# Performance work log

Measured on AMD Instinct MI355X. Metric: run time of the kernel, lower is better.

The kernel has to match this reference:

```python
import jax, jax.numpy as jnp
import numpy as np

B, S, H, FF, E = 4, 4096, 1024, 4096, 8
EPS = 1e-5


def setup_inputs() -> dict:
    key = jax.random.key(0)
    ks = jax.random.split(key, 8)
    std = 0.02
    return {
        "x": jax.random.normal(ks[0], (B, S, H), jnp.float32),
        "norm_weight": jnp.ones((H,), jnp.float32),
        "router_w": jax.random.normal(ks[1], (E, H), jnp.float32) * std,
        "router_b": jnp.zeros((E,), jnp.float32),
        "fc1_w": jax.random.normal(ks[2], (E, FF, H), jnp.float32) * std,
        "fc1_b": jnp.zeros((E, FF), jnp.float32),
        "fc2_w": jax.random.normal(ks[3], (E, H, FF), jnp.float32) * std,
        "fc2_b": jnp.zeros((E, H), jnp.float32),
    }


def reference(x, norm_weight, router_w, router_b, fc1_w, fc1_b, fc2_w, fc2_b):
    b, s, h = x.shape
    T = b * s
    e = router_w.shape[0]
    cap = T // e  # expert capacity, capacity_factor = 1.0

    x_flat = x.reshape(T, h)
    # RMSNorm (pre-norm on MoE input)
    xn = x_flat * jax.lax.rsqrt(jnp.mean(x_flat * x_flat, axis=-1, keepdims=True) + EPS) * norm_weight

    # Router (no jitter: eval / jitter_noise=0)
    logits = xn @ router_w.T + router_b          # [T, E]
    probs = jax.nn.softmax(logits, axis=-1)       # [T, E]

    # Expert-choice routing: each expert picks its top-`cap` tokens by prob
    gates, idx = jax.lax.top_k(probs.T, cap)      # [E, cap], [E, cap]

    # Dispatch (gather) and grouped expert MLP
    xe = xn[idx]                                   # [E, cap, H]
    hmid = jnp.einsum('ech,efh->ecf', xe, fc1_w) + fc1_b[:, None, :]
    hmid = jax.nn.gelu(hmid, approximate=False)    # torch F.gelu default (exact)
    ye = jnp.einsum('ecf,ehf->ech', hmid, fc2_w) + fc2_b[:, None, :]

    # Combine: gated scatter-add back to token positions, normalize by gate sum
    flat_idx = idx.reshape(-1)                     # [E*cap]
    weighted = (ye * gates[..., None]).reshape(-1, h)
    out = jnp.zeros((T, h), x.dtype).at[flat_idx].add(weighted)
    gate_sums = jnp.zeros((T, 1), x.dtype).at[flat_idx].add(gates.reshape(-1, 1))
    out = out / jnp.maximum(gate_sums, 1e-9)       # unrouted tokens stay zero
    return out.reshape(b, s, h)
```

## Files before the change

### kernel.cpp

```cpp
#include <hip/hip_runtime.h>
#include <hip/hip_bf16.h>

#define T_TOK 16384
#define H_DIM 1024
#define FF_DIM 4096
#define NE 8
#define CAP 2048
#define EPS_F 1e-5f

#define BM2 256
#define BN2 256
#define BK2 32

typedef __attribute__((ext_vector_type(4))) float f32x4;
typedef __attribute__((ext_vector_type(8))) short bf16x8;
typedef unsigned long long u64;
typedef unsigned int u32;

__device__ inline void gload_lds16(const void* g, void* l) {
  __builtin_amdgcn_global_load_lds(
      (const __attribute__((address_space(1))) unsigned int*)g,
      (__attribute__((address_space(3))) unsigned int*)l, 16, 0, 0);
}

__device__ inline unsigned short bf16_bits(float f) {
  __hip_bfloat16 h = __float2bfloat16(f);
  unsigned short u;
  __builtin_memcpy(&u, &h, 2);
  return u;
}

__device__ inline float bits_f32(unsigned short u) {
  const u32 x = ((u32)u) << 16;
  float f;
  __builtin_memcpy(&f, &x, 4);
  return f;
}

__global__ __launch_bounds__(256) void router_kernel(
    const float* __restrict__ x, const float* __restrict__ nw,
    const float* __restrict__ rw, const float* __restrict__ rb,
    __hip_bfloat16* __restrict__ xn, u64* __restrict__ keys,
    int* __restrict__ tok_cnt,
    const float* __restrict__ w1s, __hip_bfloat16* __restrict__ w1d,
    const float* __restrict__ w2s, __hip_bfloat16* __restrict__ w2d, int do_cvt) {
  const int t = blockIdx.x;
  const int tid = threadIdx.x;
  if (tid == 0) tok_cnt[t] = 0;
  const float4 v = reinterpret_cast<const float4*>(x + (size_t)t * H_DIM)[tid];
  float ss = v.x * v.x + v.y * v.y + v.z * v.z + v.w * v.w;
#pragma unroll
  for (int o = 32; o > 0; o >>= 1) ss += __shfl_down(ss, o);
  __shared__ float red[4];
  __shared__ float redl[4][NE];
  const int wv = tid >> 6, ln = tid & 63;
  if (ln == 0) red[wv] = ss;
  __syncthreads();
  const float tot = red[0] + red[1] + red[2] + red[3];
  const float scale = rsqrtf(tot * (1.0f / H_DIM) + EPS_F);
  const float4 w4 = reinterpret_cast<const float4*>(nw)[tid];
  float xv0 = v.x * scale * w4.x, xv1 = v.y * scale * w4.y;
  float xv2 = v.z * scale * w4.z, xv3 = v.w * scale * w4.w;
  ushort4 u4;
  u4.x = bf16_bits(xv0); u4.y = bf16_bits(xv1);
  u4.z = bf16_bits(xv2); u4.w = bf16_bits(xv3);
  reinterpret_cast<ushort4*>(xn + (size_t)t * H_DIM)[tid] = u4;
  float lg[NE];
#pragma unroll
  for (int e = 0; e < NE; ++e) {
    const float4 r4 = reinterpret_cast<const float4*>(rw + (size_t)e * H_DIM)[tid];
    lg[e] = xv0 * r4.x + xv1 * r4.y + xv2 * r4.z + xv3 * r4.w;
  }
#pragma unroll
  for (int o = 32; o > 0; o >>= 1) {
#pragma unroll
    for (int e = 0; e < NE; ++e) lg[e] += __shfl_down(lg[e], o);
  }
  if (ln == 0) {
#pragma unroll
    for (int e = 0; e < NE; ++e) redl[wv][e] = lg[e];
  }
  __syncthreads();
  if (tid == 0) {
    float l[NE];
    float m = -1e30f;
#pragma unroll
    for (int e = 0; e < NE; ++e) {
      l[e] = redl[0][e] + redl[1][e] + redl[2][e] + redl[3][e] + rb[e];
      m = fmaxf(m, l[e]);
    }
    float s = 0.f;
#pragma unroll
    for (int e = 0; e < NE; ++e) { l[e] = expf(l[e] - m); s += l[e]; }
    const float inv = 1.0f / s;
#pragma unroll
    for (int e = 0; e < NE; ++e) {
      const float p = l[e] * inv;
      const u64 key = ((u64)__float_as_uint(p) << 32) | (u32)(0xFFFFFFFFu - (u32)t);
      keys[(size_t)e * T_TOK + t] = key;
    }
  }
  if (do_cvt) {
    const int n4each = NE * FF_DIM * H_DIM / 4;
    const int gstride = gridDim.x * blockDim.x;
    for (int i = blockIdx.x * blockDim.x + tid; i < 2 * n4each; i += gstride) {
      const float* s = (i < n4each) ? w1s : w2s;
      __hip_bfloat16* d = (i < n4each) ? w1d : w2d;
      const int j = (i < n4each) ? i : i - n4each;
      const float4 vv = reinterpret_cast<const float4*>(s)[j];
      ushort4 o;
      o.x = bf16_bits(vv.x); o.y = bf16_bits(vv.y);
      o.z = bf16_bits(vv.z); o.w = bf16_bits(vv.w);
      reinterpret_cast<ushort4*>(d)[j] = o;
    }
  }
}

#define EQCAP 7168
__global__ __launch_bounds__(1024) void topk_kernel(
    const u64* __restrict__ keys, int* __restrict__ idxl,
    float* __restrict__ gatel, int* __restrict__ tok_list, int* __restrict__ tok_cnt) {
  const int e = blockIdx.x;
  const int tid = threadIdx.x;
  const int lane = tid & 63;
  const u64* ke = keys + (size_t)e * T_TOK;
  __shared__ int hist[256];
  __shared__ u32 s_pref;
  __shared__ int s_k;
  __shared__ int s_cnt;
  __shared__ int s_eq;
  __shared__ u32 eqlist[EQCAP];

  u32 pref = 0;
  int pbits = 0;
  int kneed = CAP;
  for (int pass = 0; pass < 4; ++pass) {
    if (tid < 256) hist[tid] = 0;
    __syncthreads();
    const int shift = 24 - 8 * pass;
    for (int i = tid; i < T_TOK; i += 1024) {
      const u32 hi = (u32)(ke[i] >> 32);
      const bool ok = (pbits == 0) || ((hi >> (32 - pbits)) == pref);
      const int d = ok ? (int)((hi >> shift) & 255) : -1;
      u64 act = __ballot(ok);
      while (act) {
        const int src = __ffsll((long long)act) - 1;
        const int dl = __shfl(d, src);
        const u64 mb = __ballot(ok && (d == dl));
        if (lane == src) atomicAdd(&hist[dl], (int)__popcll(mb));
        act &= ~mb;
      }
    }
    __syncthreads();
    if (tid == 0) {
      int cum = 0;
      int d = 255;
      for (; d >= 0; --d) {
        cum += hist[d];
        if (cum >= kneed) break;
      }
      s_k = kneed - (cum - hist[d]);
      s_pref = (pref << 8) | (u32)d;
    }
    __syncthreads();
    pref = s_pref;
    kneed = s_k;
    pbits += 8;
    __syncthreads();
  }
  const u32 thrp = pref;
  const float thrp_f = __uint_as_float(thrp);

  if (tid == 0) { s_cnt = 0; s_eq = 0; }
  __syncthreads();
  for (int i = tid; i < T_TOK; i += 1024) {
    const u64 key = ke[i];
    const u32 hi = (u32)(key >> 32);
    if (hi > thrp) {
      const int pos = atomicAdd(&s_cnt, 1);
      if (pos < CAP) {
        const int tok = (int)(0xFFFFFFFFu - (u32)key);
        idxl[e * CAP + pos] = tok;
        gatel[e * CAP + pos] = __uint_as_float(hi);
        const int j = atomicAdd(tok_cnt + tok, 1);
        if (j < NE) tok_list[tok * NE + j] = e * CAP + pos;
      }
    } else if (hi == thrp) {
      const int j = atomicAdd(&s_eq, 1);
      if (j < EQCAP) eqlist[j] = (u32)key;
    }
  }
  __syncthreads();
  const int neq = s_eq;
  if (neq <= EQCAP) {
    u32 prefl = 0;
    int pb = 0;
    int kn = kneed;
    if (neq > kneed) {
      for (int pass = 0; pass < 4; ++pass) {
        if (tid < 256) hist[tid] = 0;
        __syncthreads();
        const int shift = 24 - 8 * pass;
        for (int i = tid; i < neq; i += 1024) {
          const u32 vv = eqlist[i];
          if ((pb == 0) || ((vv >> (32 - pb)) == prefl)) atomicAdd(&hist[(vv >> shift) & 255], 1);
        }
        __syncthreads();
        if (tid == 0) {
          int cum = 0;
          int d = 255;
          for (; d >= 0; --d) {
            cum += hist[d];
            if (cum >= kn) break;
          }
          s_k = kn - (cum - hist[d]);
          s_pref = (prefl << 8) | (u32)d;
        }
        __syncthreads();
        prefl = s_pref;
        kn = s_k;
        pb += 8;
        __syncthreads();
      }
    }
    for (int i = tid; i < neq; i += 1024) {
      const u32 lo = eqlist[i];
      if (neq <= kneed || lo >= prefl) {
        const int pos = atomicAdd(&s_cnt, 1);
        if (pos < CAP) {
          const int tok = (int)(0xFFFFFFFFu - lo);
          idxl[e * CAP + pos] = tok;
          gatel[e * CAP + pos] = thrp_f;
          const int j = atomicAdd(tok_cnt + tok, 1);
          if (j < NE) tok_list[tok * NE + j] = e * CAP + pos;
        }
      }
    }
  } else {
    u64 pref64 = (u64)thrp;
    int pb64 = 32;
    int kn = kneed;
    for (int pass = 4; pass < 8; ++pass) {
      if (tid < 256) hist[tid] = 0;
      __syncthreads();
      const int shift = 56 - 8 * pass;
      for (int i = tid; i < T_TOK; i += 1024) {
        const u64 key = ke[i];
        if ((key >> (64 - pb64)) == pref64) atomicAdd(&hist[(int)((key >> shift) & 255)], 1);
      }
      __syncthreads();
      if (tid == 0) {
        int cum = 0;
        int d = 255;
        for (; d >= 0; --d) {
          cum += hist[d];
          if (cum >= kn) break;
        }
        s_k = kn - (cum - hist[d]);
        s_pref = (u32)d;
      }
      __syncthreads();
      pref64 = (pref64 << 8) | s_pref;
      kn = s_k;
      pb64 += 8;
      __syncthreads();
    }
    for (int i = tid; i < T_TOK; i += 1024) {
      const u64 key = ke[i];
      if ((u32)(key >> 32) == thrp && key >= pref64) {
        const int pos = atomicAdd(&s_cnt, 1);
        if (pos < CAP) {
          const int tok = (int)(0xFFFFFFFFu - (u32)key);
          idxl[e * CAP + pos] = tok;
          gatel[e * CAP + pos] = thrp_f;
          const int j = atomicAdd(tok_cnt + tok, 1);
          if (j < NE) tok_list[tok * NE + j] = e * CAP + pos;
        }
      }
    }
  }
}

__global__ __launch_bounds__(256) void cvt2_kernel(
    const float* __restrict__ s1, __hip_bfloat16* __restrict__ d1,
    const float* __restrict__ s2, __hip_bfloat16* __restrict__ d2, int n4each) {
  int i = blockIdx.x * blockDim.x + threadIdx.x;
  const int stride = gridDim.x * blockDim.x;
  for (; i < 2 * n4each; i += stride) {
    const float* s = (i < n4each) ? s1 : s2;
    __hip_bfloat16* d = (i < n4each) ? d1 : d2;
    const int j = (i < n4each) ? i : i - n4each;
    const float4 v = reinterpret_cast<const float4*>(s)[j];
    ushort4 o;
    o.x = bf16_bits(v.x); o.y = bf16_bits(v.y);
    o.z = bf16_bits(v.z); o.w = bf16_bits(v.w);
    reinterpret_cast<ushort4*>(d)[j] = o;
  }
}

template <int MODE>
__global__ __launch_bounds__(1024) void gemm7_kernel(
    const __hip_bfloat16* __restrict__ Asrc, const __hip_bfloat16* __restrict__ Bw,
    const float* __restrict__ bias, const int* __restrict__ idxl,
    const float* __restrict__ gatel, __hip_bfloat16* __restrict__ hmid,
    __hip_bfloat16* __restrict__ ye, int ebase) {
  constexpr int N = (MODE == 0) ? FF_DIM : H_DIM;
  constexpr int K = (MODE == 0) ? H_DIM : FF_DIM;
  constexpr int NBN = N / BN2;
  constexpr int LOG_NBN = (MODE == 0) ? 4 : 2;
  constexpr int BPE = (CAP / BM2) * NBN;
  constexpr int LOG_BPE = (MODE == 0) ? 7 : 5;
  constexpr int NT = K / BK2;

  const int nwg = gridDim.x;
  const int wg0 = blockIdx.x;
  const int wg = (wg0 & 7) * (nwg >> 3) + (wg0 >> 3);
  const int z = wg >> LOG_BPE;
  const int rr = wg & (BPE - 1);
  const int bm = rr >> LOG_NBN;
  const int bn = rr & (NBN - 1);
  const int e = ebase + z;

  const int tid = threadIdx.x;
  const int lane = tid & 63;
  const int w = tid >> 6;
  const int wr = w >> 2, wc = w & 3;
  const int fr = lane & 15, q = lane >> 4;

  __shared__ char smem[131072];

  const int srow = tid >> 2;
  const int sg = tid & 3;
  const int skoff = (sg ^ ((srow >> 1) & 3)) * 8;

  const __hip_bfloat16* asrc;
  if constexpr (MODE == 0) {
    const int t0 = idxl[e * CAP + bm * BM2 + srow];
    asrc = Asrc + (size_t)t0 * H_DIM + skoff;
  } else {
    asrc = Asrc + ((size_t)z * CAP + bm * BM2 + srow) * FF_DIM + skoff;
  }
  const __hip_bfloat16* bsrc = Bw + (size_t)z * N * K + (size_t)(bn * BN2 + srow) * K + skoff;

  const int slotk = ((q ^ ((fr >> 1) & 3)) << 4);
  const int aoff0 = (wr * 64 + fr) * 64 + slotk;
  const int boff0 = 16384 + (wc * 64 + fr) * 64 + slotk;

  f32x4 acc[4][4] = {};
  bf16x8 Af[4], Bf[4];

#define GLDA(sb, k0) gload_lds16(asrc + (k0), smem + (sb)*32768 + tid * 16)
#define GLDB(sb, k0) gload_lds16(bsrc + (k0), smem + (sb)*32768 + 16384 + tid * 16)

  GLDA(0, 0); GLDB(0, 0);
  GLDA(1, BK2); GLDB(1, BK2);
  GLDA(2, 2 * BK2); GLDB(2, 2 * BK2);
  asm volatile("s_waitcnt vmcnt(4)");
  __builtin_amdgcn_s_barrier();
  __builtin_amdgcn_sched_barrier(0);

  for (int kt = 0; kt < NT; ++kt) {
    const int cur = kt & 3;
    const int kref = (kt + 3 < NT) ? (kt + 3) : (kt + 3 - NT);
    const int k0p = kref * BK2;
    const int psl = (kt + 3) & 3;
    const char* base = smem + cur * 32768;

    Af[0] = *reinterpret_cast<const bf16x8*>(base + aoff0);
    Af[1] = *reinterpret_cast<const bf16x8*>(base + aoff0 + 1024);
    Af[2] = *reinterpret_cast<const bf16x8*>(base + aoff0 + 2048);
    Af[3] = *reinterpret_cast<const bf16x8*>(base + aoff0 + 3072);
    Bf[0] = *reinterpret_cast<const bf16x8*>(base + boff0);
    Bf[1] = *reinterpret_cast<const bf16x8*>(base + boff0 + 1024);
    __builtin_amdgcn_sched_barrier(0);
    Bf[2] = *reinterpret_cast<const bf16x8*>(base + boff0 + 2048);
    Bf[3] = *reinterpret_cast<const bf16x8*>(base + boff0 + 3072);
    GLDA(psl, k0p);
    asm volatile("s_waitcnt vmcnt(3)");
    __builtin_amdgcn_s_barrier();
    asm volatile("s_waitcnt lgkmcnt(2)");
    __builtin_amdgcn_sched_barrier(0);
    __builtin_amdgcn_s_setprio(1);
#pragma unroll
    for (int m_ = 0; m_ < 4; ++m_) {
      acc[m_][0] = __builtin_amdgcn_mfma_f32_16x16x32_bf16(Af[m_], Bf[0], acc[m_][0], 0, 0, 0);
      acc[m_][1] = __builtin_amdgcn_mfma_f32_16x16x32_bf16(Af[m_], Bf[1], acc[m_][1], 0, 0, 0);
    }
    __builtin_amdgcn_s_setprio(0);
    __builtin_amdgcn_sched_barrier(0);

    GLDB(psl, k0p);
    asm volatile("s_waitcnt lgkmcnt(0)");
    __builtin_amdgcn_sched_barrier(0);
    __builtin_amdgcn_s_barrier();
    __builtin_amdgcn_sched_barrier(0);
    __builtin_amdgcn_s_setprio(1);
#pragma unroll
    for (int m_ = 0; m_ < 4; ++m_) {
      acc[m_][2] = __builtin_amdgcn_mfma_f32_16x16x32_bf16(Af[m_], Bf[2], acc[m_][2], 0, 0, 0);
      acc[m_][3] = __builtin_amdgcn_mfma_f32_16x16x32_bf16(Af[m_], Bf[3], acc[m_][3], 0, 0, 0);
    }
    __builtin_amdgcn_s_setprio(0);
    __builtin_amdgcn_sched_barrier(0);
  }
#undef GLDA
#undef GLDB

  if constexpr (MODE == 0) {
#pragma unroll
    for (int m = 0; m < 4; ++m) {
      const int rbase = bm * BM2 + wr * 64 + m * 16 + q * 4;
#pragma unroll
      for (int n = 0; n < 4; ++n) {
        const int gn = bn * BN2 + wc * 64 + n * 16 + fr;
        const float bb = bias[e * FF_DIM + gn];
#pragma unroll
        for (int i = 0; i < 4; ++i) {
          const float v = acc[m][n][i] + bb;
          const float u = v * (1.5957691216f + 0.0713548162972f * v * v);
          const float s = 1.0f / (1.0f + __expf(-u));
          hmid[((size_t)z * CAP + rbase + i) * FF_DIM + gn] = __float2bfloat16(v * s);
        }
      }
    }
  } else {
#pragma unroll
    for (int m = 0; m < 4; ++m) {
      const int rbase = bm * BM2 + wr * 64 + m * 16 + q * 4;
      float gt[4];
#pragma unroll
      for (int i = 0; i < 4; ++i) gt[i] = gatel[e * CAP + rbase + i];
#pragma unroll
      for (int n = 0; n < 4; ++n) {
        const int gn = bn * BN2 + wc * 64 + n * 16 + fr;
        const float bb = bias[e * H_DIM + gn];
#pragma unroll
        for (int i = 0; i < 4; ++i)
          ye[((size_t)e * CAP + rbase + i) * H_DIM + gn] =
              __float2bfloat16((acc[m][n][i] + bb) * gt[i]);
      }
    }
  }
}

__global__ __launch_bounds__(256) void combine_kernel(
    const __hip_bfloat16* __restrict__ ye, const float* __restrict__ gatel,
    const int* __restrict__ tok_list, const int* __restrict__ tok_cnt,
    float* __restrict__ out) {
  const int t = blockIdx.x;
  const int tid = threadIdx.x;
  const int cnt = tok_cnt[t];
  float a0 = 0.f, a1 = 0.f, a2 = 0.f, a3 = 0.f, gs = 0.f;
  for (int j = 0; j < cnt && j < NE; ++j) {
    const int ent = tok_list[t * NE + j];
    gs += gatel[ent];
    const ushort4 v = reinterpret_cast<const ushort4*>(ye + (size_t)ent * H_DIM)[tid];
    a0 += bits_f32(v.x);
    a1 += bits_f32(v.y);
    a2 += bits_f32(v.z);
    a3 += bits_f32(v.w);
  }
  const float inv = 1.0f / fmaxf(gs, 1e-9f);
  float4 o;
  o.x = a0 * inv; o.y = a1 * inv; o.z = a2 * inv; o.w = a3 * inv;
  reinterpret_cast<float4*>(out + (size_t)t * H_DIM)[tid] = o;
}

extern "C" void kernel_launch(void* const* d_in, const int* in_sizes, int n_in,
                              void* d_out, int out_size, void* d_ws, size_t ws_size,
                              hipStream_t stream) {
  const float* x = (const float*)d_in[0];
  const float* nw = (const float*)d_in[1];
  const float* rw = (const float*)d_in[2];
  const float* rb = (const float*)d_in[3];
  const float* fc1w = (const float*)d_in[4];
  const float* fc1b = (const float*)d_in[5];
  const float* fc2w = (const float*)d_in[6];
  const float* fc2b = (const float*)d_in[7];
  float* out = (float*)d_out;

  char* ws = (char*)d_ws;
  size_t off = 0;
  auto alloc = [&](size_t b) {
    char* p = ws + off;
    off += (b + 255) & ~(size_t)255;
    return p;
  };
  __hip_bfloat16* xn = (__hip_bfloat16*)alloc((size_t)T_TOK * H_DIM * 2);
  u64* keys = (u64*)alloc((size_t)NE * T_TOK * 8);
  int* idxl = (int*)alloc((size_t)NE * CAP * 4);
  float* gatel = (float*)alloc((size_t)NE * CAP * 4);
  int* tok_list = (int*)alloc((size_t)T_TOK * NE * 4);
  int* tok_cnt = (int*)alloc((size_t)T_TOK * 4);
  __hip_bfloat16* ye = (__hip_bfloat16*)alloc((size_t)NE * CAP * H_DIM * 2);

  int EC = NE;
  while (EC > 1) {
    const size_t per = (size_t)EC * ((size_t)FF_DIM * H_DIM * 2 * 2 + (size_t)CAP * FF_DIM * 2);
    if (off + per + 4096 <= ws_size) break;
    EC >>= 1;
  }
  __hip_bfloat16* w1b = (__hip_bfloat16*)alloc((size_t)EC * FF_DIM * H_DIM * 2);
  __hip_bfloat16* w2b = (__hip_bfloat16*)alloc((size_t)EC * H_DIM * FF_DIM * 2);
  __hip_bfloat16* hmid = (__hip_bfloat16*)alloc((size_t)EC * CAP * FF_DIM * 2);

  const int fused_cvt = (EC == NE) ? 1 : 0;

  router_kernel<<<T_TOK, 256, 0, stream>>>(x, nw, rw, rb, xn, keys, tok_cnt,
                                           fc1w, w1b, fc2w, w2b, fused_cvt);
  topk_kernel<<<NE, 1024, 0, stream>>>(keys, idxl, gatel, tok_list, tok_cnt);

  for (int eb = 0; eb < NE; eb += EC) {
    if (!fused_cvt) {
      const int n4 = EC * FF_DIM * H_DIM / 4;
      cvt2_kernel<<<4096, 256, 0, stream>>>(fc1w + (size_t)eb * FF_DIM * H_DIM, w1b,
                                            fc2w + (size_t)eb * H_DIM * FF_DIM, w2b, n4);
    }
    const int nb1 = EC * (CAP / BM2) * (FF_DIM / BN2);
    gemm7_kernel<0><<<nb1, 1024, 0, stream>>>(xn, w1b, fc1b, idxl, gatel, hmid, ye, eb);
    const int nb2 = EC * (CAP / BM2) * (H_DIM / BN2);
    gemm7_kernel<1><<<nb2, 1024, 0, stream>>>(hmid, w2b, fc2b, idxl, gatel, hmid, ye, eb);
  }
  combine_kernel<<<T_TOK, 256, 0, stream>>>(ye, gatel, tok_list, tok_cnt, out);
}
```

Before: 505.3 us.

## Shrink expert GEMM tiles to 256x128 with 512 threads and triple-buffered LDS

Replaces the 1024-thread 256x256 expert GEMM with a 512-thread 256x128 tile. Each thread now loads two A rows per stage, and the LDS ring drops from four stages to three, cutting shared memory to 72KB. The aim is to run more workgroups per CU and launch twice as many blocks, which should improve latency hiding and load balance. In exchange, each B tile is reused across fewer columns, so more global traffic goes to the A operand, and the shallower prefetch may expose more memory latency.

```diff
diff --git a/kernel.cpp b/kernel.cpp
--- a/kernel.cpp
+++ b/kernel.cpp
@@ -8,8 +8,8 @@
 #define CAP 2048
 #define EPS_F 1e-5f
 
-#define BM2 256
-#define BN2 256
+#define BM3 256
+#define BN3 128
 #define BK2 32
 
 typedef __attribute__((ext_vector_type(4))) float f32x4;
@@ -299,17 +299,17 @@
 }
 
 template <int MODE>
-__global__ __launch_bounds__(1024) void gemm7_kernel(
+__global__ __launch_bounds__(512, 4) void gemm10_kernel(
     const __hip_bfloat16* __restrict__ Asrc, const __hip_bfloat16* __restrict__ Bw,
     const float* __restrict__ bias, const int* __restrict__ idxl,
     const float* __restrict__ gatel, __hip_bfloat16* __restrict__ hmid,
     __hip_bfloat16* __restrict__ ye, int ebase) {
   constexpr int N = (MODE == 0) ? FF_DIM : H_DIM;
   constexpr int K = (MODE == 0) ? H_DIM : FF_DIM;
-  constexpr int NBN = N / BN2;
-  constexpr int LOG_NBN = (MODE == 0) ? 4 : 2;
-  constexpr int BPE = (CAP / BM2) * NBN;
-  constexpr int LOG_BPE = (MODE == 0) ? 7 : 5;
+  constexpr int NBN = N / BN3;
+  constexpr int LOG_NBN = (MODE == 0) ? 5 : 3;
+  constexpr int BPE = (CAP / BM3) * NBN;
+  constexpr int LOG_BPE = (MODE == 0) ? 8 : 6;
   constexpr int NT = K / BK2;
 
   const int nwg = gridDim.x;
@@ -324,23 +324,27 @@
   const int tid = threadIdx.x;
   const int lane = tid & 63;
   const int w = tid >> 6;
-  const int wr = w >> 2, wc = w & 3;
+  const int wr = w >> 1, wc = w & 1;
   const int fr = lane & 15, q = lane >> 4;
 
-  __shared__ char smem[131072];
+  __shared__ char smem[73728];
 
   const int srow = tid >> 2;
   const int sg = tid & 3;
   const int skoff = (sg ^ ((srow >> 1) & 3)) * 8;
 
-  const __hip_bfloat16* asrc;
+  const __hip_bfloat16* asrc0;
+  const __hip_bfloat16* asrc1;
   if constexpr (MODE == 0) {
-    const int t0 = idxl[e * CAP + bm * BM2 + srow];
-    asrc = Asrc + (size_t)t0 * H_DIM + skoff;
+    const int t0 = idxl[e * CAP + bm * BM3 + srow];
+    const int t1 = idxl[e * CAP + bm * BM3 + 128 + srow];
+    asrc0 = Asrc + (size_t)t0 * H_DIM + skoff;
+    asrc1 = Asrc + (size_t)t1 * H_DIM + skoff;
   } else {
-    asrc = Asrc + ((size_t)z * CAP + bm * BM2 + srow) * FF_DIM + skoff;
-  }
-  const __hip_bfloat16* bsrc = Bw + (size_t)z * N * K + (size_t)(bn * BN2 + srow) * K + skoff;
+    asrc0 = Asrc + ((size_t)z * CAP + bm * BM3 + srow) * FF_DIM + skoff;
+    asrc1 = asrc0 + (size_t)128 * FF_DIM;
+  }
+  const __hip_bfloat16* bsrc = Bw + (size_t)z * N * K + (size_t)(bn * BN3 + srow) * K + skoff;
 
   const int slotk = ((q ^ ((fr >> 1) & 3)) << 4);
   const int aoff0 = (wr * 64 + fr) * 64 + slotk;
@@ -349,22 +353,26 @@
   f32x4 acc[4][4] = {};
   bf16x8 Af[4], Bf[4];
 
-#define GLDA(sb, k0) gload_lds16(asrc + (k0), smem + (sb)*32768 + tid * 16)
-#define GLDB(sb, k0) gload_lds16(bsrc + (k0), smem + (sb)*32768 + 16384 + tid * 16)
+#define GLDA(sb, k0)                                            \
+  do {                                                          \
+    char* d_ = smem + (sb)*24576 + tid * 16;                    \
+    gload_lds16(asrc0 + (k0), d_);                              \
+    gload_lds16(asrc1 + (k0), d_ + 8192);                       \
+  } while (0)
+#define GLDB(sb, k0) gload_lds16(bsrc + (k0), smem + (sb)*24576 + 16384 + tid * 16)
 
   GLDA(0, 0); GLDB(0, 0);
   GLDA(1, BK2); GLDB(1, BK2);
-  GLDA(2, 2 * BK2); GLDB(2, 2 * BK2);
-  asm volatile("s_waitcnt vmcnt(4)");
+  asm volatile("s_waitcnt vmcnt(3)");
   __builtin_amdgcn_s_barrier();
   __builtin_amdgcn_sched_barrier(0);
 
   for (int kt = 0; kt < NT; ++kt) {
-    const int cur = kt & 3;
-    const int kref = (kt + 3 < NT) ? (kt + 3) : (kt + 3 - NT);
+    const int cur = kt % 3;
+    const int psl = (kt + 2) % 3;
+    const int kref = (kt + 2 < NT) ? (kt + 2) : (kt + 2 - NT);
     const int k0p = kref * BK2;
-    const int psl = (kt + 3) & 3;
-    const char* base = smem + cur * 32768;
+    const char* base = smem + cur * 24576;
 
     Af[0] = *reinterpret_cast<const bf16x8*>(base + aoff0);
     Af[1] = *reinterpret_cast<const bf16x8*>(base + aoff0 + 1024);
@@ -376,7 +384,7 @@
     Bf[2] = *reinterpret_cast<const bf16x8*>(base + boff0 + 2048);
     Bf[3] = *reinterpret_cast<const bf16x8*>(base + boff0 + 3072);
     GLDA(psl, k0p);
-    asm volatile("s_waitcnt vmcnt(3)");
+    asm volatile("s_waitcnt vmcnt(2)");
     __builtin_amdgcn_s_barrier();
     asm volatile("s_waitcnt lgkmcnt(2)");
     __builtin_amdgcn_sched_barrier(0);
@@ -409,10 +417,10 @@
   if constexpr (MODE == 0) {
 #pragma unroll
     for (int m = 0; m < 4; ++m) {
-      const int rbase = bm * BM2 + wr * 64 + m * 16 + q * 4;
+      const int rbase = bm * BM3 + wr * 64 + m * 16 + q * 4;
 #pragma unroll
       for (int n = 0; n < 4; ++n) {
-        const int gn = bn * BN2 + wc * 64 + n * 16 + fr;
+        const int gn = bn * BN3 + wc * 64 + n * 16 + fr;
         const float bb = bias[e * FF_DIM + gn];
 #pragma unroll
         for (int i = 0; i < 4; ++i) {
@@ -426,13 +434,13 @@
   } else {
 #pragma unroll
     for (int m = 0; m < 4; ++m) {
-      const int rbase = bm * BM2 + wr * 64 + m * 16 + q * 4;
+      const int rbase = bm * BM3 + wr * 64 + m * 16 + q * 4;
       float gt[4];
 #pragma unroll
       for (int i = 0; i < 4; ++i) gt[i] = gatel[e * CAP + rbase + i];
 #pragma unroll
       for (int n = 0; n < 4; ++n) {
-        const int gn = bn * BN2 + wc * 64 + n * 16 + fr;
+        const int gn = bn * BN3 + wc * 64 + n * 16 + fr;
         const float bb = bias[e * H_DIM + gn];
 #pragma unroll
         for (int i = 0; i < 4; ++i)
@@ -516,10 +524,10 @@
       cvt2_kernel<<<4096, 256, 0, stream>>>(fc1w + (size_t)eb * FF_DIM * H_DIM, w1b,
                                             fc2w + (size_t)eb * H_DIM * FF_DIM, w2b, n4);
     }
-    const int nb1 = EC * (CAP / BM2) * (FF_DIM / BN2);
-    gemm7_kernel<0><<<nb1, 1024, 0, stream>>>(xn, w1b, fc1b, idxl, gatel, hmid, ye, eb);
-    const int nb2 = EC * (CAP / BM2) * (H_DIM / BN2);
-    gemm7_kernel<1><<<nb2, 1024, 0, stream>>>(hmid, w2b, fc2b, idxl, gatel, hmid, ye, eb);
+    const int nb1 = EC * (CAP / BM3) * (FF_DIM / BN3);
+    gemm10_kernel<0><<<nb1, 512, 0, stream>>>(xn, w1b, fc1b, idxl, gatel, hmid, ye, eb);
+    const int nb2 = EC * (CAP / BM3) * (H_DIM / BN3);
+    gemm10_kernel<1><<<nb2, 512, 0, stream>>>(hmid, w2b, fc2b, idxl, gatel, hmid, ye, eb);
   }
   combine_kernel<<<T_TOK, 256, 0, stream>>>(ye, gatel, tok_list, tok_cnt, out);
 }
```

New measurement: 540.1 us. +6.9%, slower.

## Restructure expert GEMMs to 512 threads, BK=64, 128x64 warp tiles, double buffering

Applied to the files above, without the earlier changes.

Rewrites the grouped expert GEMM kernel so it uses 8 waves of 512 threads instead of 16, each computing a 128x64 sub-tile with 8x4 accumulators. The K step doubles to 64 and the pipeline changes from a 4-stage ring of 32-wide tiles to two 64 KB buffers with a new XOR swizzle. LDS fragment reads are interleaved with MFMA groups. The aim is to raise MFMA work per LDS read and per barrier, at the cost of higher register pressure and a shallower prefetch depth.

```diff
diff --git a/kernel.cpp b/kernel.cpp
--- a/kernel.cpp
+++ b/kernel.cpp
@@ -10,7 +10,7 @@
 
 #define BM2 256
 #define BN2 256
-#define BK2 32
+#define BK3 64
 
 typedef __attribute__((ext_vector_type(4))) float f32x4;
 typedef __attribute__((ext_vector_type(8))) short bf16x8;
@@ -299,7 +299,7 @@
 }
 
 template <int MODE>
-__global__ __launch_bounds__(1024) void gemm7_kernel(
+__global__ __launch_bounds__(512) void gemm12_kernel(
     const __hip_bfloat16* __restrict__ Asrc, const __hip_bfloat16* __restrict__ Bw,
     const float* __restrict__ bias, const int* __restrict__ idxl,
     const float* __restrict__ gatel, __hip_bfloat16* __restrict__ hmid,
@@ -310,7 +310,7 @@
   constexpr int LOG_NBN = (MODE == 0) ? 4 : 2;
   constexpr int BPE = (CAP / BM2) * NBN;
   constexpr int LOG_BPE = (MODE == 0) ? 7 : 5;
-  constexpr int NT = K / BK2;
+  constexpr int NT = K / BK3;
 
   const int nwg = gridDim.x;
   const int wg0 = blockIdx.x;
@@ -329,87 +329,132 @@
 
   __shared__ char smem[131072];
 
-  const int srow = tid >> 2;
-  const int sg = tid & 3;
-  const int skoff = (sg ^ ((srow >> 1) & 3)) * 8;
-
-  const __hip_bfloat16* asrc;
+  const int srow = tid >> 3;
+  const int sg = tid & 7;
+  const int skoff = (sg ^ (srow & 7)) * 8;
+
+  const __hip_bfloat16* as0;
+  const __hip_bfloat16* as1;
+  const __hip_bfloat16* as2;
+  const __hip_bfloat16* as3;
   if constexpr (MODE == 0) {
-    const int t0 = idxl[e * CAP + bm * BM2 + srow];
-    asrc = Asrc + (size_t)t0 * H_DIM + skoff;
+    as0 = Asrc + (size_t)idxl[e * CAP + bm * BM2 + srow] * H_DIM + skoff;
+    as1 = Asrc + (size_t)idxl[e * CAP + bm * BM2 + 64 + srow] * H_DIM + skoff;
+    as2 = Asrc + (size_t)idxl[e * CAP + bm * BM2 + 128 + srow] * H_DIM + skoff;
+    as3 = Asrc + (size_t)idxl[e * CAP + bm * BM2 + 192 + srow] * H_DIM + skoff;
   } else {
-    asrc = Asrc + ((size_t)z * CAP + bm * BM2 + srow) * FF_DIM + skoff;
-  }
-  const __hip_bfloat16* bsrc = Bw + (size_t)z * N * K + (size_t)(bn * BN2 + srow) * K + skoff;
-
-  const int slotk = ((q ^ ((fr >> 1) & 3)) << 4);
-  const int aoff0 = (wr * 64 + fr) * 64 + slotk;
-  const int boff0 = 16384 + (wc * 64 + fr) * 64 + slotk;
-
-  f32x4 acc[4][4] = {};
-  bf16x8 Af[4], Bf[4];
-
-#define GLDA(sb, k0) gload_lds16(asrc + (k0), smem + (sb)*32768 + tid * 16)
-#define GLDB(sb, k0) gload_lds16(bsrc + (k0), smem + (sb)*32768 + 16384 + tid * 16)
-
-  GLDA(0, 0); GLDB(0, 0);
-  GLDA(1, BK2); GLDB(1, BK2);
-  GLDA(2, 2 * BK2); GLDB(2, 2 * BK2);
-  asm volatile("s_waitcnt vmcnt(4)");
+    as0 = Asrc + ((size_t)z * CAP + bm * BM2 + srow) * FF_DIM + skoff;
+    as1 = as0 + (size_t)64 * FF_DIM;
+    as2 = as0 + (size_t)128 * FF_DIM;
+    as3 = as0 + (size_t)192 * FF_DIM;
+  }
+  const __hip_bfloat16* bs0 = Bw + (size_t)z * N * K + (size_t)(bn * BN2 + srow) * K + skoff;
+  const __hip_bfloat16* bs1 = bs0 + (size_t)64 * K;
+  const __hip_bfloat16* bs2 = bs0 + (size_t)128 * K;
+  const __hip_bfloat16* bs3 = bs0 + (size_t)192 * K;
+
+  int aoffk[2], boffk[2];
+#pragma unroll
+  for (int ks = 0; ks < 2; ++ks) {
+    aoffk[ks] = (wr * 128 + fr) * 128 + (((ks * 4 + q) ^ (fr & 7)) << 4);
+    boffk[ks] = 32768 + (wc * 64 + fr) * 128 + (((ks * 4 + q) ^ (fr & 7)) << 4);
+  }
+
+  f32x4 acc[8][4] = {};
+  bf16x8 Bf[8], Aa[4], Ab[4];
+
+#define STAGE12(buf, kt)                                     \
+  do {                                                       \
+    const int k0_ = (kt)*BK3;                                \
+    char* d_ = smem + (buf)*65536 + tid * 16;                \
+    gload_lds16(as0 + k0_, d_);                              \
+    gload_lds16(as1 + k0_, d_ + 8192);                       \
+    gload_lds16(as2 + k0_, d_ + 16384);                      \
+    gload_lds16(as3 + k0_, d_ + 24576);                      \
+    gload_lds16(bs0 + k0_, d_ + 32768);                      \
+    gload_lds16(bs1 + k0_, d_ + 40960);                      \
+    gload_lds16(bs2 + k0_, d_ + 49152);                      \
+    gload_lds16(bs3 + k0_, d_ + 57344);                      \
+  } while (0)
+
+#define RDA(F, m0_)                                                                  \
+  do {                                                                              \
+    F[0] = *reinterpret_cast<const bf16x8*>(base + (m0_)*2048 + aoffk[0]);          \
+    F[1] = *reinterpret_cast<const bf16x8*>(base + (m0_)*2048 + aoffk[1]);          \
+    F[2] = *reinterpret_cast<const bf16x8*>(base + (m0_ + 1) * 2048 + aoffk[0]);    \
+    F[3] = *reinterpret_cast<const bf16x8*>(base + (m0_ + 1) * 2048 + aoffk[1]);    \
+  } while (0)
+
+#define MM16(F, m0_)                                                                           \
+  do {                                                                                         \
+    _Pragma("unroll") for (int n_ = 0; n_ < 4; ++n_) {                                         \
+      acc[m0_][n_] = __builtin_amdgcn_mfma_f32_16x16x32_bf16(F[0], Bf[n_ * 2], acc[m0_][n_], 0, 0, 0); \
+      acc[m0_][n_] = __builtin_amdgcn_mfma_f32_16x16x32_bf16(F[1], Bf[n_ * 2 + 1], acc[m0_][n_], 0, 0, 0); \
+      acc[m0_ + 1][n_] = __builtin_amdgcn_mfma_f32_16x16x32_bf16(F[2], Bf[n_ * 2], acc[m0_ + 1][n_], 0, 0, 0); \
+      acc[m0_ + 1][n_] = __builtin_amdgcn_mfma_f32_16x16x32_bf16(F[3], Bf[n_ * 2 + 1], acc[m0_ + 1][n_], 0, 0, 0); \
+    }                                                                                          \
+  } while (0)
+
+  STAGE12(0, 0);
+  STAGE12(1, 1);
+  asm volatile("s_waitcnt vmcnt(8)");
   __builtin_amdgcn_s_barrier();
   __builtin_amdgcn_sched_barrier(0);
 
   for (int kt = 0; kt < NT; ++kt) {
-    const int cur = kt & 3;
-    const int kref = (kt + 3 < NT) ? (kt + 3) : (kt + 3 - NT);
-    const int k0p = kref * BK2;
-    const int psl = (kt + 3) & 3;
-    const char* base = smem + cur * 32768;
-
-    Af[0] = *reinterpret_cast<const bf16x8*>(base + aoff0);
-    Af[1] = *reinterpret_cast<const bf16x8*>(base + aoff0 + 1024);
-    Af[2] = *reinterpret_cast<const bf16x8*>(base + aoff0 + 2048);
-    Af[3] = *reinterpret_cast<const bf16x8*>(base + aoff0 + 3072);
-    Bf[0] = *reinterpret_cast<const bf16x8*>(base + boff0);
-    Bf[1] = *reinterpret_cast<const bf16x8*>(base + boff0 + 1024);
-    __builtin_amdgcn_sched_barrier(0);
-    Bf[2] = *reinterpret_cast<const bf16x8*>(base + boff0 + 2048);
-    Bf[3] = *reinterpret_cast<const bf16x8*>(base + boff0 + 3072);
-    GLDA(psl, k0p);
-    asm volatile("s_waitcnt vmcnt(3)");
+    const char* base = smem + (kt & 1) * 65536;
+#pragma unroll
+    for (int n_ = 0; n_ < 4; ++n_) {
+      Bf[n_ * 2] = *reinterpret_cast<const bf16x8*>(base + n_ * 2048 + boffk[0]);
+      Bf[n_ * 2 + 1] = *reinterpret_cast<const bf16x8*>(base + n_ * 2048 + boffk[1]);
+    }
+    RDA(Aa, 0);
+    __builtin_amdgcn_sched_barrier(0);
+    RDA(Ab, 2);
+    __builtin_amdgcn_sched_barrier(0);
+    asm volatile("s_waitcnt lgkmcnt(4)");
+    __builtin_amdgcn_sched_barrier(0);
+    __builtin_amdgcn_s_setprio(1);
+    MM16(Aa, 0);
+    __builtin_amdgcn_s_setprio(0);
+    __builtin_amdgcn_sched_barrier(0);
+    RDA(Aa, 4);
+    __builtin_amdgcn_sched_barrier(0);
+    asm volatile("s_waitcnt lgkmcnt(4)");
+    __builtin_amdgcn_sched_barrier(0);
+    __builtin_amdgcn_s_setprio(1);
+    MM16(Ab, 2);
+    __builtin_amdgcn_s_setprio(0);
+    __builtin_amdgcn_sched_barrier(0);
+    RDA(Ab, 6);
+    __builtin_amdgcn_sched_barrier(0);
+    asm volatile("s_waitcnt lgkmcnt(4)");
+    __builtin_amdgcn_sched_barrier(0);
+    __builtin_amdgcn_s_setprio(1);
+    MM16(Aa, 4);
+    __builtin_amdgcn_s_setprio(0);
+    __builtin_amdgcn_sched_barrier(0);
+    asm volatile("s_waitcnt lgkmcnt(0)");
+    __builtin_amdgcn_sched_barrier(0);
+    __builtin_amdgcn_s_setprio(1);
+    MM16(Ab, 6);
+    __builtin_amdgcn_s_setprio(0);
+    __builtin_amdgcn_sched_barrier(0);
     __builtin_amdgcn_s_barrier();
-    asm volatile("s_waitcnt lgkmcnt(2)");
-    __builtin_amdgcn_sched_barrier(0);
-    __builtin_amdgcn_s_setprio(1);
-#pragma unroll
-    for (int m_ = 0; m_ < 4; ++m_) {
-      acc[m_][0] = __builtin_amdgcn_mfma_f32_16x16x32_bf16(Af[m_], Bf[0], acc[m_][0], 0, 0, 0);
-      acc[m_][1] = __builtin_amdgcn_mfma_f32_16x16x32_bf16(Af[m_], Bf[1], acc[m_][1], 0, 0, 0);
-    }
-    __builtin_amdgcn_s_setprio(0);
-    __builtin_amdgcn_sched_barrier(0);
-
-    GLDB(psl, k0p);
-    asm volatile("s_waitcnt lgkmcnt(0)");
-    __builtin_amdgcn_sched_barrier(0);
+    const int kref = (kt + 2 < NT) ? (kt + 2) : (kt + 2 - NT);
+    STAGE12(kt & 1, kref);
+    asm volatile("s_waitcnt vmcnt(8)");
     __builtin_amdgcn_s_barrier();
     __builtin_amdgcn_sched_barrier(0);
-    __builtin_amdgcn_s_setprio(1);
-#pragma unroll
-    for (int m_ = 0; m_ < 4; ++m_) {
-      acc[m_][2] = __builtin_amdgcn_mfma_f32_16x16x32_bf16(Af[m_], Bf[2], acc[m_][2], 0, 0, 0);
-      acc[m_][3] = __builtin_amdgcn_mfma_f32_16x16x32_bf16(Af[m_], Bf[3], acc[m_][3], 0, 0, 0);
-    }
-    __builtin_amdgcn_s_setprio(0);
-    __builtin_amdgcn_sched_barrier(0);
-  }
-#undef GLDA
-#undef GLDB
+  }
+#undef STAGE12
+#undef RDA
+#undef MM16
 
   if constexpr (MODE == 0) {
 #pragma unroll
-    for (int m = 0; m < 4; ++m) {
-      const int rbase = bm * BM2 + wr * 64 + m * 16 + q * 4;
+    for (int m = 0; m < 8; ++m) {
+      const int rbase = bm * BM2 + wr * 128 + m * 16 + q * 4;
 #pragma unroll
       for (int n = 0; n < 4; ++n) {
         const int gn = bn * BN2 + wc * 64 + n * 16 + fr;
@@ -425,8 +470,8 @@
     }
   } else {
 #pragma unroll
-    for (int m = 0; m < 4; ++m) {
-      const int rbase = bm * BM2 + wr * 64 + m * 16 + q * 4;
+    for (int m = 0; m < 8; ++m) {
+      const int rbase = bm * BM2 + wr * 128 + m * 16 + q * 4;
       float gt[4];
 #pragma unroll
       for (int i = 0; i < 4; ++i) gt[i] = gatel[e * CAP + rbase + i];
@@ -517,9 +562,9 @@
                                             fc2w + (size_t)eb * H_DIM * FF_DIM, w2b, n4);
     }
     const int nb1 = EC * (CAP / BM2) * (FF_DIM / BN2);
-    gemm7_kernel<0><<<nb1, 1024, 0, stream>>>(xn, w1b, fc1b, idxl, gatel, hmid, ye, eb);
+    gemm12_kernel<0><<<nb1, 512, 0, stream>>>(xn, w1b, fc1b, idxl, gatel, hmid, ye, eb);
     const int nb2 = EC * (CAP / BM2) * (H_DIM / BN2);
-    gemm7_kernel<1><<<nb2, 1024, 0, stream>>>(hmid, w2b, fc2b, idxl, gatel, hmid, ye, eb);
+    gemm12_kernel<1><<<nb2, 512, 0, stream>>>(hmid, w2b, fc2b, idxl, gatel, hmid, ye, eb);
   }
   combine_kernel<<<T_TOK, 256, 0, stream>>>(ye, gatel, tok_list, tok_cnt, out);
 }
```

New measurement: 537.4 us. +6.3%, slower.

## Switch expert GEMMs to 32x32x16 MFMA with k-split LDS layout

Applied to the files above, without the earlier changes.

Replaces the 16x16x32 bf16 MFMA tiling (4x4 fragments per wave) with 32x32x16 MFMA (2x2 fragments per wave). The LDS staging layout is reorganised into two k-halves of 16 elements each, with the XOR swizzle dropped, and the epilogue is rewritten for the 32x32 accumulator row mapping. The aim is fewer LDS fragment loads and instructions per k-step and a more efficient MFMA shape. The unswizzled layout risks LDS bank conflicts, and the new epilogue writes narrower column patterns.

```diff
diff --git a/kernel.cpp b/kernel.cpp
--- a/kernel.cpp
+++ b/kernel.cpp
@@ -13,6 +13,7 @@
 #define BK2 32
 
 typedef __attribute__((ext_vector_type(4))) float f32x4;
+typedef __attribute__((ext_vector_type(16))) float f32x16;
 typedef __attribute__((ext_vector_type(8))) short bf16x8;
 typedef unsigned long long u64;
 typedef unsigned int u32;
@@ -299,7 +300,7 @@
 }
 
 template <int MODE>
-__global__ __launch_bounds__(1024) void gemm7_kernel(
+__global__ __launch_bounds__(1024) void gemm13_kernel(
     const __hip_bfloat16* __restrict__ Asrc, const __hip_bfloat16* __restrict__ Bw,
     const float* __restrict__ bias, const int* __restrict__ idxl,
     const float* __restrict__ gatel, __hip_bfloat16* __restrict__ hmid,
@@ -325,29 +326,36 @@
   const int lane = tid & 63;
   const int w = tid >> 6;
   const int wr = w >> 2, wc = w & 3;
-  const int fr = lane & 15, q = lane >> 4;
+  const int l31 = lane & 31;
+  const int hi = lane >> 5;
 
   __shared__ char smem[131072];
 
-  const int srow = tid >> 2;
-  const int sg = tid & 3;
-  const int skoff = (sg ^ ((srow >> 1) & 3)) * 8;
+  const int skh = tid >> 9;
+  const int srow = (tid >> 1) & 255;
+  const int shq = tid & 1;
+  const int selem = skh * 16 + shq * 8;
 
   const __hip_bfloat16* asrc;
   if constexpr (MODE == 0) {
     const int t0 = idxl[e * CAP + bm * BM2 + srow];
-    asrc = Asrc + (size_t)t0 * H_DIM + skoff;
+    asrc = Asrc + (size_t)t0 * H_DIM + selem;
   } else {
-    asrc = Asrc + ((size_t)z * CAP + bm * BM2 + srow) * FF_DIM + skoff;
-  }
-  const __hip_bfloat16* bsrc = Bw + (size_t)z * N * K + (size_t)(bn * BN2 + srow) * K + skoff;
-
-  const int slotk = ((q ^ ((fr >> 1) & 3)) << 4);
-  const int aoff0 = (wr * 64 + fr) * 64 + slotk;
-  const int boff0 = 16384 + (wc * 64 + fr) * 64 + slotk;
-
-  f32x4 acc[4][4] = {};
-  bf16x8 Af[4], Bf[4];
+    asrc = Asrc + ((size_t)z * CAP + bm * BM2 + srow) * FF_DIM + selem;
+  }
+  const __hip_bfloat16* bsrc = Bw + (size_t)z * N * K + (size_t)(bn * BN2 + srow) * K + selem;
+
+  int aoff[2][2], boff[2][2];
+#pragma unroll
+  for (int mt = 0; mt < 2; ++mt)
+#pragma unroll
+    for (int ks = 0; ks < 2; ++ks) {
+      aoff[mt][ks] = ks * 8192 + (wr * 64 + mt * 32 + l31) * 32 + hi * 16;
+      boff[mt][ks] = 16384 + ks * 8192 + (wc * 64 + mt * 32 + l31) * 32 + hi * 16;
+    }
+
+  f32x16 acc00 = {}, acc01 = {}, acc10 = {}, acc11 = {};
+  bf16x8 A0k0, A1k0, B0k0, B1k0, A0k1, A1k1, B0k1, B1k1;
 
 #define GLDA(sb, k0) gload_lds16(asrc + (k0), smem + (sb)*32768 + tid * 16)
 #define GLDB(sb, k0) gload_lds16(bsrc + (k0), smem + (sb)*32768 + 16384 + tid * 16)
@@ -366,26 +374,25 @@
     const int psl = (kt + 3) & 3;
     const char* base = smem + cur * 32768;
 
-    Af[0] = *reinterpret_cast<const bf16x8*>(base + aoff0);
-    Af[1] = *reinterpret_cast<const bf16x8*>(base + aoff0 + 1024);
-    Af[2] = *reinterpret_cast<const bf16x8*>(base + aoff0 + 2048);
-    Af[3] = *reinterpret_cast<const bf16x8*>(base + aoff0 + 3072);
-    Bf[0] = *reinterpret_cast<const bf16x8*>(base + boff0);
-    Bf[1] = *reinterpret_cast<const bf16x8*>(base + boff0 + 1024);
+    A0k0 = *reinterpret_cast<const bf16x8*>(base + aoff[0][0]);
+    A1k0 = *reinterpret_cast<const bf16x8*>(base + aoff[1][0]);
+    B0k0 = *reinterpret_cast<const bf16x8*>(base + boff[0][0]);
+    B1k0 = *reinterpret_cast<const bf16x8*>(base + boff[1][0]);
     __builtin_amdgcn_sched_barrier(0);
-    Bf[2] = *reinterpret_cast<const bf16x8*>(base + boff0 + 2048);
-    Bf[3] = *reinterpret_cast<const bf16x8*>(base + boff0 + 3072);
+    A0k1 = *reinterpret_cast<const bf16x8*>(base + aoff[0][1]);
+    A1k1 = *reinterpret_cast<const bf16x8*>(base + aoff[1][1]);
+    B0k1 = *reinterpret_cast<const bf16x8*>(base + boff[0][1]);
+    B1k1 = *reinterpret_cast<const bf16x8*>(base + boff[1][1]);
     GLDA(psl, k0p);
     asm volatile("s_waitcnt vmcnt(3)");
     __builtin_amdgcn_s_barrier();
-    asm volatile("s_waitcnt lgkmcnt(2)");
+    asm volatile("s_waitcnt lgkmcnt(4)");
     __builtin_amdgcn_sched_barrier(0);
     __builtin_amdgcn_s_setprio(1);
-#pragma unroll
-    for (int m_ = 0; m_ < 4; ++m_) {
-      acc[m_][0] = __builtin_amdgcn_mfma_f32_16x16x32_bf16(Af[m_], Bf[0], acc[m_][0], 0, 0, 0);
-      acc[m_][1] = __builtin_amdgcn_mfma_f32_16x16x32_bf16(Af[m_], Bf[1], acc[m_][1], 0, 0, 0);
-    }
+    acc00 = __builtin_amdgcn_mfma_f32_32x32x16_bf16(A0k0, B0k0, acc00, 0, 0, 0);
+    acc01 = __builtin_amdgcn_mfma_f32_32x32x16_bf16(A0k0, B1k0, acc01, 0, 0, 0);
+    acc10 = __builtin_amdgcn_mfma_f32_32x32x16_bf16(A1k0, B0k0, acc10, 0, 0, 0);
+    acc11 = __builtin_amdgcn_mfma_f32_32x32x16_bf16(A1k0, B1k0, acc11, 0, 0, 0);
     __builtin_amdgcn_s_setprio(0);
     __builtin_amdgcn_sched_barrier(0);
 
@@ -395,52 +402,40 @@
     __builtin_amdgcn_s_barrier();
     __builtin_amdgcn_sched_barrier(0);
     __builtin_amdgcn_s_setprio(1);
-#pragma unroll
-    for (int m_ = 0; m_ < 4; ++m_) {
-      acc[m_][2] = __builtin_amdgcn_mfma_f32_16x16x32_bf16(Af[m_], Bf[2], acc[m_][2], 0, 0, 0);
-      acc[m_][3] = __builtin_amdgcn_mfma_f32_16x16x32_bf16(Af[m_], Bf[3], acc[m_][3], 0, 0, 0);
-    }
+    acc00 = __builtin_amdgcn_mfma_f32_32x32x16_bf16(A0k1, B0k1, acc00, 0, 0, 0);
+    acc01 = __builtin_amdgcn_mfma_f32_32x32x16_bf16(A0k1, B1k1, acc01, 0, 0, 0);
+    acc10 = __builtin_amdgcn_mfma_f32_32x32x16_bf16(A1k1, B0k1, acc10, 0, 0, 0);
+    acc11 = __builtin_amdgcn_mfma_f32_32x32x16_bf16(A1k1, B1k1, acc11, 0, 0, 0);
     __builtin_amdgcn_s_setprio(0);
     __builtin_amdgcn_sched_barrier(0);
   }
 #undef GLDA
 #undef GLDB
 
-  if constexpr (MODE == 0) {
-#pragma unroll
-    for (int m = 0; m < 4; ++m) {
-      const int rbase = bm * BM2 + wr * 64 + m * 16 + q * 4;
-#pragma unroll
-      for (int n = 0; n < 4; ++n) {
-        const int gn = bn * BN2 + wc * 64 + n * 16 + fr;
-        const float bb = bias[e * FF_DIM + gn];
-#pragma unroll
-        for (int i = 0; i < 4; ++i) {
-          const float v = acc[m][n][i] + bb;
-          const float u = v * (1.5957691216f + 0.0713548162972f * v * v);
-          const float s = 1.0f / (1.0f + __expf(-u));
-          hmid[((size_t)z * CAP + rbase + i) * FF_DIM + gn] = __float2bfloat16(v * s);
-        }
-      }
-    }
-  } else {
-#pragma unroll
-    for (int m = 0; m < 4; ++m) {
-      const int rbase = bm * BM2 + wr * 64 + m * 16 + q * 4;
-      float gt[4];
-#pragma unroll
-      for (int i = 0; i < 4; ++i) gt[i] = gatel[e * CAP + rbase + i];
-#pragma unroll
-      for (int n = 0; n < 4; ++n) {
-        const int gn = bn * BN2 + wc * 64 + n * 16 + fr;
-        const float bb = bias[e * H_DIM + gn];
-#pragma unroll
-        for (int i = 0; i < 4; ++i)
-          ye[((size_t)e * CAP + rbase + i) * H_DIM + gn] =
-              __float2bfloat16((acc[m][n][i] + bb) * gt[i]);
-      }
-    }
-  }
+#define EPI(accv, mt, nt)                                                               \
+  do {                                                                                  \
+    const int gcol = bn * BN2 + wc * 64 + (nt)*32 + l31;                                \
+    const float bb = bias[e * ((MODE == 0) ? FF_DIM : H_DIM) + gcol];                   \
+    _Pragma("unroll") for (int r_ = 0; r_ < 16; ++r_) {                                 \
+      const int grow = bm * BM2 + wr * 64 + (mt)*32 + (r_ & 3) + 8 * (r_ >> 2) + 4 * hi;\
+      if constexpr (MODE == 0) {                                                        \
+        const float v_ = accv[r_] + bb;                                                 \
+        const float u_ = v_ * (1.5957691216f + 0.0713548162972f * v_ * v_);             \
+        const float s_ = 1.0f / (1.0f + __expf(-u_));                                   \
+        hmid[((size_t)z * CAP + grow) * FF_DIM + gcol] = __float2bfloat16(v_ * s_);     \
+      } else {                                                                          \
+        const float gt_ = gatel[e * CAP + grow];                                        \
+        ye[((size_t)e * CAP + grow) * H_DIM + gcol] =                                   \
+            __float2bfloat16((accv[r_] + bb) * gt_);                                    \
+      }                                                                                 \
+    }                                                                                   \
+  } while (0)
+
+  EPI(acc00, 0, 0);
+  EPI(acc01, 0, 1);
+  EPI(acc10, 1, 0);
+  EPI(acc11, 1, 1);
+#undef EPI
 }
 
 __global__ __launch_bounds__(256) void combine_kernel(
@@ -517,9 +512,9 @@
                                             fc2w + (size_t)eb * H_DIM * FF_DIM, w2b, n4);
     }
     const int nb1 = EC * (CAP / BM2) * (FF_DIM / BN2);
-    gemm7_kernel<0><<<nb1, 1024, 0, stream>>>(xn, w1b, fc1b, idxl, gatel, hmid, ye, eb);
+    gemm13_kernel<0><<<nb1, 1024, 0, stream>>>(xn, w1b, fc1b, idxl, gatel, hmid, ye, eb);
     const int nb2 = EC * (CAP / BM2) * (H_DIM / BN2);
-    gemm7_kernel<1><<<nb2, 1024, 0, stream>>>(hmid, w2b, fc2b, idxl, gatel, hmid, ye, eb);
+    gemm13_kernel<1><<<nb2, 1024, 0, stream>>>(hmid, w2b, fc2b, idxl, gatel, hmid, ye, eb);
   }
   combine_kernel<<<T_TOK, 256, 0, stream>>>(ye, gatel, tok_list, tok_cnt, out);
 }
```

Result: slower. 566.4 us (+12.1%).
